# Kernel tuning notes

Hardware: AMD Instinct MI355X
Metric: run time of the kernel (lower is better)

Reference implementation:

```python
import jax, jax.numpy as jnp
import numpy as np

B, S, D, H = 2, 2048, 1024, 16
MAX_DIST = 1024


def setup_inputs() -> dict:
    key = jax.random.key(0)
    ks = jax.random.split(key, 7)
    w = lambda k, shape: jax.random.normal(k, shape, jnp.float32) * 0.02
    return {
        "x": jax.random.normal(ks[0], (B, S, D), jnp.float32),
        "Wq": w(ks[1], (D, D)), "bq": jnp.zeros((D,), jnp.float32),
        "Wk": w(ks[2], (D, D)),
        "Wv": w(ks[3], (D, D)), "bv": jnp.zeros((D,), jnp.float32),
        "Wo": w(ks[4], (D, D)), "bo": jnp.zeros((D,), jnp.float32),
        "pos_bias": w(ks[5], (2 * MAX_DIST - 1, H)),
        "max_dist": MAX_DIST,
    }


def reference(x, Wq, bq, Wk, Wv, bv, Wo, bo, pos_bias, max_dist):
    b, s, d_model = x.shape
    h = pos_bias.shape[1]
    hd = d_model // h  # head dim
    scale = hd ** -0.25  # module's scale applied to (QK^T + rel_bias)

    split = lambda t: t.reshape(b, s, h, hd).transpose(0, 2, 1, 3)  # [b,h,s,hd]
    q = split(x @ Wq + bq)
    k = split(x @ Wk)          # key has no bias
    v = split(x @ Wv + bv)

    # raw QK^T (unscaled), as in the module
    scores = jnp.einsum('bhqd,bhkd->bhqk', q, k)

    # relative-position bias gather: clamp(i-j) -> table index
    pos = jnp.arange(s)[:, None] - jnp.arange(s)[None, :]
    pos = jnp.clip(pos, -max_dist + 1, max_dist - 1) + max_dist - 1
    rel_bias = pos_bias[pos].transpose(2, 0, 1)[None]  # [1,h,s,s]

    # SDPA with attn_mask = (scores + rel_bias)*scale adds it on top of QK^T/sqrt(hd)
    logits = scores * (1.0 / jnp.sqrt(jnp.float32(hd))) + (scores + rel_bias) * scale
    w = jax.nn.softmax(logits, axis=-1)

    out = jnp.einsum('bhqk,bhkd->bhqd', w, v)
    out = out.transpose(0, 2, 1, 3).reshape(b, s, d_model)
    return out @ Wo + bo
```

## Files before the change

### kernel.cpp

```cpp
#include <hip/hip_runtime.h>
#include <hip/hip_bf16.h>
#include <cstddef>
#include <cstdint>

#define BATCH   2
#define S_LEN   2048
#define D_MODEL 1024
#define NH      16
#define HD      64
#define MAXD    1024

#define SCORE_SCALE 0.47855339059327373f
#define BIAS_SCALE  0.35355339059327373f
#define FIXM 8.0f
#define LOG2E 1.4426950408889634f

typedef __attribute__((ext_vector_type(8))) short bf16x8;
typedef __attribute__((ext_vector_type(4))) float f32x4;

static __device__ __forceinline__ unsigned short f2bf(float f) {
    __hip_bfloat16 h = __float2bfloat16(f);
    return *reinterpret_cast<unsigned short*>(&h);
}
static __device__ __forceinline__ float bf2f(unsigned short u) {
    union { unsigned int i; float f; } c;
    c.i = ((unsigned int)u) << 16;
    return c.f;
}

#define GLDS(gp, lp) __builtin_amdgcn_global_load_lds( \
    (const __attribute__((address_space(1))) void*)(gp), \
    (__attribute__((address_space(3))) void*)(lp), 16, 0, 0)

__global__ __launch_bounds__(256) void prep(
    const float* __restrict__ x,
    const float* __restrict__ Wq, const float* __restrict__ Wk,
    const float* __restrict__ Wv, const float* __restrict__ Wo,
    const float* __restrict__ pos_bias,
    unsigned short* __restrict__ xb, unsigned short* __restrict__ Wqkvt,
    unsigned short* __restrict__ Wot_hi, unsigned short* __restrict__ Wot_lo,
    float* __restrict__ pb_t)
{
    __shared__ float t[32][33];
    const int bx = blockIdx.x, tid = threadIdx.x;

    if (bx < 2048) {
        const size_t i = ((size_t)bx * 256 + tid) * 8;
        const float4 a = *(const float4*)(x + i);
        const float4 b = *(const float4*)(x + i + 4);
        unsigned short u[8] = {f2bf(a.x), f2bf(a.y), f2bf(a.z), f2bf(a.w),
                               f2bf(b.x), f2bf(b.y), f2bf(b.z), f2bf(b.w)};
        *(uint4*)(xb + i) = *(const uint4*)u;
    } else if (bx < 6144) {
        const int bx2 = bx - 2048;
        const int z = bx2 >> 10, inner = bx2 & 1023;
        const int gx = inner & 31, gy = inner >> 5;
        const float* W = (z == 0) ? Wq : (z == 1) ? Wk : (z == 2) ? Wv : Wo;
        unsigned short* hi = (z < 3) ? Wqkvt + (size_t)z * 1024 * 1024 : Wot_hi;
        unsigned short* lo = (z == 3) ? Wot_lo : nullptr;
        const int bxx = gx * 32, byy = gy * 32;
        const int tx = tid & 31, ty = tid >> 5;
        #pragma unroll
        for (int i = 0; i < 4; i++)
            t[ty + 8 * i][tx] = W[(size_t)(byy + ty + 8 * i) * 1024 + bxx + tx];
        __syncthreads();
        #pragma unroll
        for (int i = 0; i < 4; i++) {
            const float v = t[tx][ty + 8 * i];
            const unsigned short hh = f2bf(v);
            const size_t o = (size_t)(bxx + ty + 8 * i) * 1024 + byy + tx;
            hi[o] = hh;
            if (lo) lo[o] = f2bf(v - bf2f(hh));
        }
    } else {
        const int o0 = (bx - 6144) * 1024 + tid * 4;
        float v[4];
        #pragma unroll
        for (int j = 0; j < 4; j++) {
            const int o = o0 + j;
            const int hh = o >> 12, ii = o & 4095;
            int rel = ii - 2047;
            rel = min(max(rel, -(MAXD - 1)), MAXD - 1);
            v[j] = (BIAS_SCALE * pos_bias[(size_t)(rel + MAXD - 1) * NH + hh] - FIXM) * LOG2E;
        }
        *(float4*)&pb_t[o0] = *(const float4*)v;
    }
}

#define GBM 128
#define GBN 128
#define GBK 32

__global__ __launch_bounds__(256) void gemm_qkv(
    const unsigned short* __restrict__ A, const unsigned short* __restrict__ Bt,
    const float* __restrict__ bq, const float* __restrict__ bv,
    unsigned short* __restrict__ Cout)
{
    const int M = 4096, N = 3072, K = 1024;
    __shared__ __align__(16) unsigned short As[GBM][GBK];
    __shared__ __align__(16) unsigned short Bs[GBN][GBK];

    const int tid = threadIdx.x;
    const int wave = tid >> 6, lane = tid & 63;
    const int quad = lane >> 4, cl = lane & 15;
    const int wm = (wave & 1) * 64, wn = (wave >> 1) * 64;
    const int bm = blockIdx.y * GBM, bn = blockIdx.x * GBN;

    const int sr = wave * 32 + (lane >> 2);
    const int sc = (lane & 3) * 8;
    const unsigned short* aS0 = A  + (size_t)(bm + sr) * K + sc;
    const unsigned short* aS1 = aS0 + (size_t)16 * K;
    const unsigned short* bS0 = Bt + (size_t)(bn + sr) * K + sc;
    const unsigned short* bS1 = bS0 + (size_t)16 * K;
    unsigned short* aD0 = &As[wave * 32][0];
    unsigned short* aD1 = &As[wave * 32 + 16][0];
    unsigned short* bD0 = &Bs[wave * 32][0];
    unsigned short* bD1 = &Bs[wave * 32 + 16][0];

    f32x4 acc[4][4];
    #pragma unroll
    for (int mi = 0; mi < 4; mi++)
        #pragma unroll
        for (int ni = 0; ni < 4; ni++)
            #pragma unroll
            for (int r = 0; r < 4; r++) acc[mi][ni][r] = 0.f;

    for (int k0 = 0; k0 < K; k0 += GBK) {
        __syncthreads();
        GLDS(aS0, aD0); GLDS(aS1, aD1);
        GLDS(bS0, bD0); GLDS(bS1, bD1);
        aS0 += GBK; aS1 += GBK; bS0 += GBK; bS1 += GBK;
        __syncthreads();

        bf16x8 af[4], bf[4];
        #pragma unroll
        for (int mi = 0; mi < 4; mi++)
            af[mi] = *(const bf16x8*)&As[wm + mi * 16 + cl][quad * 8];
        #pragma unroll
        for (int ni = 0; ni < 4; ni++)
            bf[ni] = *(const bf16x8*)&Bs[wn + ni * 16 + cl][quad * 8];
        #pragma unroll
        for (int mi = 0; mi < 4; mi++)
            #pragma unroll
            for (int ni = 0; ni < 4; ni++)
                acc[mi][ni] = __builtin_amdgcn_mfma_f32_16x16x32_bf16(
                    af[mi], bf[ni], acc[mi][ni], 0, 0, 0);
    }

    #pragma unroll
    for (int ni = 0; ni < 4; ni++) {
        const int coln = bn + wn + ni * 16 + cl;
        const int region = coln >> 10, c = coln & 1023;
        const float bs = (region == 0) ? bq[c] : (region == 2) ? bv[c] : 0.f;
        #pragma unroll
        for (int mi = 0; mi < 4; mi++) {
            const int row0 = bm + wm + mi * 16 + quad * 4;
            if (region == 2) {
                const int hh = c >> 6, d = c & 63;
                const int bb = row0 >> 11, s0 = row0 & 2047;
                unsigned short u[4];
                #pragma unroll
                for (int r = 0; r < 4; r++) u[r] = f2bf(acc[mi][ni][r] + bs);
                unsigned short* dst = Cout + (size_t)8 * 1024 * 1024
                    + (((size_t)bb * NH + hh) * HD + d) * S_LEN + s0;
                *(uint2*)dst = *(const uint2*)u;
            } else {
                unsigned short* dst = Cout + (size_t)region * 4 * 1024 * 1024;
                #pragma unroll
                for (int r = 0; r < 4; r++)
                    dst[(size_t)(row0 + r) * 1024 + c] = f2bf(acc[mi][ni][r] + bs);
            }
        }
    }
    (void)M; (void)N;
}

#define TQB 64
#define TKB 64

__global__ __launch_bounds__(256) void attn_mfma(
    const unsigned short* __restrict__ Q, const unsigned short* __restrict__ K,
    const unsigned short* __restrict__ VT, const float* __restrict__ pb_t,
    unsigned short* __restrict__ O)
{
    const int qt = blockIdx.x, h = blockIdx.y, b = blockIdx.z;
    const int tid  = threadIdx.x;
    const int wave = tid >> 6, lane = tid & 63;
    const int quad = lane >> 4, col = lane & 15;
    const int qbase = qt * TQB;
    const int qw = qbase + wave * 16;

    __shared__ __align__(16) unsigned short Ks[2][TKB][HD];
    __shared__ __align__(16) unsigned short Vs[2][HD][TKB];
    __shared__ __align__(16) unsigned short Ps[4][16][TKB];

    bf16x8 qf[2];
    {
        const unsigned short* qp =
            &Q[((size_t)(b * S_LEN) + qw + col) * D_MODEL + h * HD + quad * 8];
        qf[0] = *(const bf16x8*)qp;
        qf[1] = *(const bf16x8*)(qp + 32);
    }

    f32x4 accO[4];
    float lsum = 0.f;
    #pragma unroll
    for (int nb = 0; nb < 4; nb++)
        #pragma unroll
        for (int r = 0; r < 4; r++) accO[nb][r] = 0.f;

    const int s0 = tid, s1 = 256 + tid;
    const int kr0 = s0 >> 3, kj0 = (s0 & 7) ^ (kr0 & 7);
    const int kr1 = s1 >> 3, kj1 = (s1 & 7) ^ (kr1 & 7);
    const unsigned short* kS0 = K + ((size_t)(b * S_LEN) + kr0) * D_MODEL + h * HD + kj0 * 8;
    const unsigned short* kS1 = K + ((size_t)(b * S_LEN) + kr1) * D_MODEL + h * HD + kj1 * 8;
    const size_t vbase = ((size_t)(b * NH + h) * HD) * S_LEN;
    const unsigned short* vS0 = VT + vbase + (size_t)kr0 * S_LEN + kj0 * 8;
    const unsigned short* vS1 = VT + vbase + (size_t)kr1 * S_LEN + kj1 * 8;

    {
        unsigned short* kb0 = &Ks[0][0][0] + wave * 512;
        unsigned short* vb0 = &Vs[0][0][0] + wave * 512;
        GLDS(kS0, kb0); GLDS(kS1, kb0 + 2048);
        GLDS(vS0, vb0); GLDS(vS1, vb0 + 2048);
        kS0 += (size_t)TKB * D_MODEL; kS1 += (size_t)TKB * D_MODEL;
        vS0 += TKB; vS1 += TKB;
    }
    __syncthreads();

    const float* pbh = pb_t + h * 4096;
    const int ridx0 = qbase + wave * 16 + col - quad * 4 + 2047;
    const float SC2 = SCORE_SCALE * LOG2E;
    const int jsw = col & 7;

    for (int kb = 0, t = 0; kb < S_LEN; kb += TKB, t++) {
        const int p = t & 1;
        if (kb + TKB < S_LEN) {
            unsigned short* kd = &Ks[p ^ 1][0][0] + wave * 512;
            unsigned short* vd = &Vs[p ^ 1][0][0] + wave * 512;
            GLDS(kS0, kd); GLDS(kS1, kd + 2048);
            GLDS(vS0, vd); GLDS(vS1, vd + 2048);
            kS0 += (size_t)TKB * D_MODEL; kS1 += (size_t)TKB * D_MODEL;
            vS0 += TKB; vS1 += TKB;
        }

        float bias_r[16];
        const int rb = ridx0 - kb;
        #pragma unroll
        for (int nb = 0; nb < 4; nb++)
            #pragma unroll
            for (int r = 0; r < 4; r++)
                bias_r[nb * 4 + r] = pbh[rb - nb * 16 - r];

        f32x4 accS[4];
        #pragma unroll
        for (int nb = 0; nb < 4; nb++)
            #pragma unroll
            for (int r = 0; r < 4; r++) accS[nb][r] = 0.f;
        #pragma unroll
        for (int kk = 0; kk < 2; kk++)
            #pragma unroll
            for (int nb = 0; nb < 4; nb++) {
                const bf16x8 kf = *(const bf16x8*)
                    &Ks[p][nb * 16 + col][((kk * 4 + quad) ^ jsw) * 8];
                accS[nb] = __builtin_amdgcn_mfma_f32_16x16x32_bf16(kf, qf[kk], accS[nb], 0, 0, 0);
            }

        #pragma unroll
        for (int nb = 0; nb < 4; nb++) {
            float pr[4];
            #pragma unroll
            for (int r = 0; r < 4; r++) {
                pr[r] = __builtin_amdgcn_exp2f(fmaf(accS[nb][r], SC2, bias_r[nb * 4 + r]));
                lsum += pr[r];
            }
            const __hip_bfloat162 h0 = __float22bfloat162_rn(make_float2(pr[0], pr[1]));
            const __hip_bfloat162 h1 = __float22bfloat162_rn(make_float2(pr[2], pr[3]));
            uint2 w;
            w.x = *(const unsigned int*)&h0;
            w.y = *(const unsigned int*)&h1;
            const int jp = ((nb * 2 + (quad >> 1)) ^ jsw) * 8 + (quad & 1) * 4;
            *(uint2*)&Ps[wave][col][jp] = w;
        }

        #pragma unroll
        for (int kk = 0; kk < 2; kk++) {
            const bf16x8 af = *(const bf16x8*)
                &Ps[wave][col][((kk * 4 + quad) ^ jsw) * 8];
            #pragma unroll
            for (int nb = 0; nb < 4; nb++) {
                const bf16x8 vf = *(const bf16x8*)
                    &Vs[p][nb * 16 + col][((kk * 4 + quad) ^ jsw) * 8];
                accO[nb] = __builtin_amdgcn_mfma_f32_16x16x32_bf16(af, vf, accO[nb], 0, 0, 0);
            }
        }
        __syncthreads();
    }

    lsum += __shfl_xor(lsum, 16);
    lsum += __shfl_xor(lsum, 32);
    #pragma unroll
    for (int r = 0; r < 4; r++) {
        const float inv = 1.0f / __shfl(lsum, quad * 4 + r);
        const size_t row = (size_t)(b * S_LEN) + qw + quad * 4 + r;
        #pragma unroll
        for (int nb = 0; nb < 4; nb++)
            O[row * D_MODEL + h * HD + nb * 16 + col] = f2bf(accO[nb][r] * inv);
    }
}

#define OBM 64
#define OBN 128

__global__ __launch_bounds__(256) void gemm_out(
    const unsigned short* __restrict__ A, const unsigned short* __restrict__ Bhi,
    const unsigned short* __restrict__ Blo, const float* __restrict__ bias,
    float* __restrict__ Cout)
{
    const int N = 1024, Kd = 1024;
    __shared__ __align__(16) unsigned short As[OBM][GBK];
    __shared__ __align__(16) unsigned short Bs[2][OBN][GBK];

    const int tid = threadIdx.x;
    const int wave = tid >> 6, lane = tid & 63;
    const int quad = lane >> 4, cl = lane & 15;
    const int wm = (wave & 1) * 32, wn = (wave >> 1) * 64;
    const int bm = blockIdx.y * OBM, bn = blockIdx.x * OBN;

    const int ar = tid >> 2, ac = (tid & 3) * 8;
    const unsigned short* aS = A + (size_t)(bm + ar) * Kd + ac;
    const unsigned short* hS0 = Bhi + (size_t)(bn + ar) * Kd + ac;
    const unsigned short* hS1 = hS0 + (size_t)64 * Kd;
    const unsigned short* lS0 = Blo + (size_t)(bn + ar) * Kd + ac;
    const unsigned short* lS1 = lS0 + (size_t)64 * Kd;
    unsigned short* aD  = &As[0][0] + wave * 512;
    unsigned short* hD0 = &Bs[0][0][0] + wave * 512;
    unsigned short* hD1 = hD0 + 2048;
    unsigned short* lD0 = &Bs[1][0][0] + wave * 512;
    unsigned short* lD1 = lD0 + 2048;

    f32x4 acc[2][4];
    #pragma unroll
    for (int mi = 0; mi < 2; mi++)
        #pragma unroll
        for (int ni = 0; ni < 4; ni++)
            #pragma unroll
            for (int r = 0; r < 4; r++) acc[mi][ni][r] = 0.f;

    for (int k0 = 0; k0 < Kd; k0 += GBK) {
        __syncthreads();
        GLDS(aS, aD);
        GLDS(hS0, hD0); GLDS(hS1, hD1);
        GLDS(lS0, lD0); GLDS(lS1, lD1);
        aS += GBK; hS0 += GBK; hS1 += GBK; lS0 += GBK; lS1 += GBK;
        __syncthreads();

        bf16x8 af[2], bh[4];
        #pragma unroll
        for (int mi = 0; mi < 2; mi++)
            af[mi] = *(const bf16x8*)&As[wm + mi * 16 + cl][quad * 8];
        #pragma unroll
        for (int ni = 0; ni < 4; ni++)
            bh[ni] = *(const bf16x8*)&Bs[0][wn + ni * 16 + cl][quad * 8];
        #pragma unroll
        for (int mi = 0; mi < 2; mi++)
            #pragma unroll
            for (int ni = 0; ni < 4; ni++)
                acc[mi][ni] = __builtin_amdgcn_mfma_f32_16x16x32_bf16(
                    af[mi], bh[ni], acc[mi][ni], 0, 0, 0);
        #pragma unroll
        for (int ni = 0; ni < 4; ni++)
            bh[ni] = *(const bf16x8*)&Bs[1][wn + ni * 16 + cl][quad * 8];
        #pragma unroll
        for (int mi = 0; mi < 2; mi++)
            #pragma unroll
            for (int ni = 0; ni < 4; ni++)
                acc[mi][ni] = __builtin_amdgcn_mfma_f32_16x16x32_bf16(
                    af[mi], bh[ni], acc[mi][ni], 0, 0, 0);
    }

    #pragma unroll
    for (int ni = 0; ni < 4; ni++) {
        const int coln = bn + wn + ni * 16 + cl;
        const float bs = bias[coln];
        #pragma unroll
        for (int mi = 0; mi < 2; mi++) {
            const int row0 = bm + wm + mi * 16 + quad * 4;
            #pragma unroll
            for (int r = 0; r < 4; r++)
                Cout[(size_t)(row0 + r) * N + coln] = acc[mi][ni][r] + bs;
        }
    }
}

extern "C" void kernel_launch(void* const* d_in, const int* in_sizes, int n_in,
                              void* d_out, int out_size, void* d_ws, size_t ws_size,
                              hipStream_t stream)
{
    const float* x        = (const float*)d_in[0];
    const float* Wq       = (const float*)d_in[1];
    const float* bq       = (const float*)d_in[2];
    const float* Wk       = (const float*)d_in[3];
    const float* Wv       = (const float*)d_in[4];
    const float* bv       = (const float*)d_in[5];
    const float* Wo       = (const float*)d_in[6];
    const float* bo       = (const float*)d_in[7];
    const float* pos_bias = (const float*)d_in[8];
    float* out = (float*)d_out;

    const size_t ELEMS  = (size_t)BATCH * S_LEN * D_MODEL;
    const size_t WELEMS = (size_t)D_MODEL * D_MODEL;
    unsigned short* xb     = (unsigned short*)d_ws;
    unsigned short* Wqkvt  = xb + ELEMS;
    unsigned short* Wot_hi = Wqkvt + 3 * WELEMS;
    unsigned short* Wot_lo = Wot_hi + WELEMS;
    unsigned short* QKV    = Wot_lo + WELEMS;
    unsigned short* Qb     = QKV;
    unsigned short* Kb     = Qb + ELEMS;
    unsigned short* VTb    = Kb + ELEMS;
    unsigned short* Ab     = VTb + ELEMS;
    float* pb_t            = (float*)(Ab + ELEMS);

    prep<<<6208, 256, 0, stream>>>(x, Wq, Wk, Wv, Wo, pos_bias,
                                   xb, Wqkvt, Wot_hi, Wot_lo, pb_t);

    gemm_qkv<<<dim3(3072 / GBN, 4096 / GBM), 256, 0, stream>>>(
        xb, Wqkvt, bq, bv, QKV);

    attn_mfma<<<dim3(S_LEN / TQB, NH, BATCH), 256, 0, stream>>>(
        Qb, Kb, VTb, pb_t, Ab);

    gemm_out<<<dim3(1024 / OBN, 4096 / OBM), 256, 0, stream>>>(
        Ab, Wot_hi, Wot_lo, bo, out);
}
```

Measured before the change: 223.7 us.

## Keep attention probabilities in registers using 16x16x16 MFMA and compute row sums via MFMA

In the attention kernel, the softmax probability tile is no longer staged through LDS. The bf16 probabilities stay in registers and feed 16x16x16 bf16 MFMAs directly, with the operands swapped so the output is transposed. Row sums are now accumulated by an MFMA against a vector of ones instead of scalar adds and shuffles, and the output store is vectorized per row. This removes LDS writes and reads and frees LDS, but it uses twice as many smaller MFMA instructions and relies on that builtin being available.

```diff
diff --git a/kernel.cpp b/kernel.cpp
--- a/kernel.cpp
+++ b/kernel.cpp
@@ -16,7 +16,14 @@
 #define LOG2E 1.4426950408889634f
 
 typedef __attribute__((ext_vector_type(8))) short bf16x8;
+typedef __attribute__((ext_vector_type(4))) short bf16x4;
 typedef __attribute__((ext_vector_type(4))) float f32x4;
+
+#if __has_builtin(__builtin_amdgcn_mfma_f32_16x16x16bf16_1k)
+#define USE_1K 1
+#else
+#define USE_1K 0
+#endif
 
 static __device__ __forceinline__ unsigned short f2bf(float f) {
     __hip_bfloat16 h = __float2bfloat16(f);
@@ -96,7 +103,7 @@
     const float* __restrict__ bq, const float* __restrict__ bv,
     unsigned short* __restrict__ Cout)
 {
-    const int M = 4096, N = 3072, K = 1024;
+    const int K = 1024;
     __shared__ __align__(16) unsigned short As[GBM][GBK];
     __shared__ __align__(16) unsigned short Bs[GBN][GBK];
 
@@ -172,7 +179,6 @@
             }
         }
     }
-    (void)M; (void)N;
 }
 
 #define TQB 64
@@ -192,7 +198,9 @@
 
     __shared__ __align__(16) unsigned short Ks[2][TKB][HD];
     __shared__ __align__(16) unsigned short Vs[2][HD][TKB];
+#if !USE_1K
     __shared__ __align__(16) unsigned short Ps[4][16][TKB];
+#endif
 
     bf16x8 qf[2];
     {
@@ -203,11 +211,18 @@
     }
 
     f32x4 accO[4];
+    #pragma unroll
+    for (int nb = 0; nb < 4; nb++)
+        #pragma unroll
+        for (int r = 0; r < 4; r++) accO[nb][r] = 0.f;
+#if USE_1K
+    f32x4 accL;
+    #pragma unroll
+    for (int r = 0; r < 4; r++) accL[r] = 0.f;
+    const bf16x4 vone = {(short)16256, (short)16256, (short)16256, (short)16256};
+#else
     float lsum = 0.f;
-    #pragma unroll
-    for (int nb = 0; nb < 4; nb++)
-        #pragma unroll
-        for (int r = 0; r < 4; r++) accO[nb][r] = 0.f;
+#endif
 
     const int s0 = tid, s1 = 256 + tid;
     const int kr0 = s0 >> 3, kj0 = (s0 & 7) ^ (kr0 & 7);
@@ -229,7 +244,7 @@
     __syncthreads();
 
     const float* pbh = pb_t + h * 4096;
-    const int ridx0 = qbase + wave * 16 + col - quad * 4 + 2047;
+    const float* pb_lane = pbh + (qbase + wave * 16 + col - quad * 4 + 2047);
     const float SC2 = SCORE_SCALE * LOG2E;
     const int jsw = col & 7;
 
@@ -245,12 +260,11 @@
         }
 
         float bias_r[16];
-        const int rb = ridx0 - kb;
         #pragma unroll
         for (int nb = 0; nb < 4; nb++)
             #pragma unroll
             for (int r = 0; r < 4; r++)
-                bias_r[nb * 4 + r] = pbh[rb - nb * 16 - r];
+                bias_r[nb * 4 + r] = pb_lane[-(nb * 16 + r)];
 
         f32x4 accS[4];
         #pragma unroll
@@ -266,23 +280,44 @@
                 accS[nb] = __builtin_amdgcn_mfma_f32_16x16x32_bf16(kf, qf[kk], accS[nb], 0, 0, 0);
             }
 
+#if USE_1K
+        bf16x4 pf[4];
+#endif
         #pragma unroll
         for (int nb = 0; nb < 4; nb++) {
             float pr[4];
             #pragma unroll
-            for (int r = 0; r < 4; r++) {
+            for (int r = 0; r < 4; r++)
                 pr[r] = __builtin_amdgcn_exp2f(fmaf(accS[nb][r], SC2, bias_r[nb * 4 + r]));
-                lsum += pr[r];
-            }
             const __hip_bfloat162 h0 = __float22bfloat162_rn(make_float2(pr[0], pr[1]));
             const __hip_bfloat162 h1 = __float22bfloat162_rn(make_float2(pr[2], pr[3]));
             uint2 w;
             w.x = *(const unsigned int*)&h0;
             w.y = *(const unsigned int*)&h1;
+#if USE_1K
+            union { uint2 u; bf16x4 v; } cv;
+            cv.u = w;
+            pf[nb] = cv.v;
+            accL = __builtin_amdgcn_mfma_f32_16x16x16bf16_1k(vone, pf[nb], accL, 0, 0, 0);
+#else
+            #pragma unroll
+            for (int r = 0; r < 4; r++) lsum += pr[r];
             const int jp = ((nb * 2 + (quad >> 1)) ^ jsw) * 8 + (quad & 1) * 4;
             *(uint2*)&Ps[wave][col][jp] = w;
-        }
-
+#endif
+        }
+
+#if USE_1K
+        #pragma unroll
+        for (int s = 0; s < 4; s++) {
+            #pragma unroll
+            for (int nb = 0; nb < 4; nb++) {
+                const bf16x4 vf = *(const bf16x4*)
+                    &Vs[p][nb * 16 + col][(((2 * s + (quad >> 1)) ^ jsw) * 8) + (quad & 1) * 4];
+                accO[nb] = __builtin_amdgcn_mfma_f32_16x16x16bf16_1k(vf, pf[s], accO[nb], 0, 0, 0);
+            }
+        }
+#else
         #pragma unroll
         for (int kk = 0; kk < 2; kk++) {
             const bf16x8 af = *(const bf16x8*)
@@ -294,9 +329,22 @@
                 accO[nb] = __builtin_amdgcn_mfma_f32_16x16x32_bf16(af, vf, accO[nb], 0, 0, 0);
             }
         }
-        __syncthreads();
-    }
-
+#endif
+        pb_lane -= TKB;
+        __syncthreads();
+    }
+
+#if USE_1K
+    const float inv = 1.0f / accL[0];
+    const size_t row = (size_t)(b * S_LEN) + qw + col;
+    #pragma unroll
+    for (int nb = 0; nb < 4; nb++) {
+        unsigned short u[4];
+        #pragma unroll
+        for (int r = 0; r < 4; r++) u[r] = f2bf(accO[nb][r] * inv);
+        *(uint2*)&O[row * D_MODEL + h * HD + nb * 16 + quad * 4] = *(const uint2*)u;
+    }
+#else
     lsum += __shfl_xor(lsum, 16);
     lsum += __shfl_xor(lsum, 32);
     #pragma unroll
@@ -307,6 +355,7 @@
         for (int nb = 0; nb < 4; nb++)
             O[row * D_MODEL + h * HD + nb * 16 + col] = f2bf(accO[nb][r] * inv);
     }
+#endif
 }
 
 #define OBM 64
```

Measured after the change: 222.1 us. No clear change (-0.7%).
